# Kernel optimization log

Hardware: AMD Instinct MI355X
Metric: run time of the kernel (lower is better)

Reference implementation:

```python
import jax, jax.numpy as jnp
import numpy as np
import math

B, L, D_MODEL, H = 8, 3072, 1024, 16
E = D_MODEL // H                      # d_keys = d_values = 64
FACTOR = 1
TOP_K = int(FACTOR * math.log(L))     # = 8 delay taps


def setup_inputs() -> dict:
    key = jax.random.key(0)
    ks = jax.random.split(key, 11)
    s = 0.02
    return {
        "queries": jax.random.normal(ks[0], (B, L, D_MODEL), jnp.float32),
        "keys":    jax.random.normal(ks[1], (B, L, D_MODEL), jnp.float32),
        "values":  jax.random.normal(ks[2], (B, L, D_MODEL), jnp.float32),
        "Wq": jax.random.normal(ks[3], (D_MODEL, D_MODEL), jnp.float32) * s,
        "bq": jnp.zeros((D_MODEL,), jnp.float32),
        "Wk": jax.random.normal(ks[4], (D_MODEL, D_MODEL), jnp.float32) * s,
        "bk": jnp.zeros((D_MODEL,), jnp.float32),
        "Wv": jax.random.normal(ks[5], (D_MODEL, D_MODEL), jnp.float32) * s,
        "bv": jnp.zeros((D_MODEL,), jnp.float32),
        "Wo": jax.random.normal(ks[6], (D_MODEL, D_MODEL), jnp.float32) * s,
        "bo": jnp.zeros((D_MODEL,), jnp.float32),
    }


def reference(queries, keys, values, Wq, bq, Wk, bk, Wv, bv, Wo, bo):
    # Q/K/V projections -> [B, L, H, E]
    q = (queries @ Wq + bq).reshape(B, L, H, E)
    k = (keys    @ Wk + bk).reshape(B, L, H, E)
    v = (values  @ Wv + bv).reshape(B, L, H, E)

    # -> [B, H, E, L], correlate along time via FFT
    qh = q.transpose(0, 2, 3, 1)
    kh = k.transpose(0, 2, 3, 1)
    vh = v.transpose(0, 2, 3, 1)
    qf = jnp.fft.rfft(qh, axis=-1)
    kf = jnp.fft.rfft(kh, axis=-1)
    corr = jnp.fft.irfft(qf * jnp.conj(kf), n=L, axis=-1)  # [B, H, E, L]

    # per-batch top-k delay selection on head/channel-averaged correlation
    mean_value = corr.mean(axis=(1, 2))                    # [B, L]
    weights, delay = jax.lax.top_k(mean_value, TOP_K)      # [B, K]
    tmp_corr = jax.nn.softmax(weights, axis=-1)            # [B, K]

    # time-delay aggregation: circular gather per selected delay, weighted sum
    init_index = jnp.arange(L)
    agg = jnp.zeros_like(vh)
    for i in range(TOP_K):  # small static loop over top-k taps
        idx = (init_index[None, :] + delay[:, i:i + 1]) % L            # [B, L]
        idx4 = jnp.broadcast_to(idx[:, None, None, :], vh.shape)       # [B,H,E,L]
        pattern = jnp.take_along_axis(vh, idx4, axis=-1)
        agg = agg + pattern * tmp_corr[:, i][:, None, None, None]

    # back to [B, L, H*E], output projection
    V = agg.transpose(0, 3, 1, 2).reshape(B, L, H * E)
    return V @ Wo + bo
```

## Files before the change

### kernel.cpp

```cpp
#include <hip/hip_runtime.h>
#include <math.h>

#define BSZ 8
#define LEN 3072
#define DM 1024
#define TOPK 8

typedef __attribute__((ext_vector_type(8))) short short8;
typedef __attribute__((ext_vector_type(4))) float f32x4;

__device__ __forceinline__ unsigned short f2bf(float x) {
    unsigned int u = __builtin_bit_cast(unsigned int, x);
    u += 0x7fffu + ((u >> 16) & 1u);
    return (unsigned short)(u >> 16);
}
__device__ __forceinline__ float bf2f(unsigned short h) {
    unsigned int u = ((unsigned int)h) << 16;
    return __builtin_bit_cast(float, u);
}
__device__ __forceinline__ void gl_lds16(const void* g, void* l) {
    __builtin_amdgcn_global_load_lds(
        (const __attribute__((address_space(1))) unsigned int*)g,
        (__attribute__((address_space(3))) unsigned int*)l, 16, 0, 0);
}

#define GBM 128
#define GBN 128
#define GBK 16

__global__ __launch_bounds__(256) void gemm_f32(const float* __restrict__ A,
    const float* __restrict__ B, float* __restrict__ C, int M, int N, int K)
{
    __shared__ float As[GBK][GBM];
    __shared__ float Bs[GBK][GBN];
    const int tid = threadIdx.x;
    const int tx = tid & 15, ty = tid >> 4;
    const size_t m0 = (size_t)blockIdx.y * GBM;
    const size_t n0 = (size_t)blockIdx.x * GBN;
    const int arow = tid >> 2, acol = (tid & 3) << 2;
    const int brow = tid >> 5, bcol = (tid & 31) << 2;

    float acc[8][8];
#pragma unroll
    for (int i = 0; i < 8; i++)
#pragma unroll
        for (int j = 0; j < 8; j++) acc[i][j] = 0.f;

    const float* Ap0 = A + (m0 + arow) * (size_t)K + acol;
    const float* Ap1 = A + (m0 + arow + 64) * (size_t)K + acol;
    const float* Bp0 = B + (size_t)brow * N + n0 + bcol;
    const float* Bp1 = B + (size_t)(brow + 8) * N + n0 + bcol;

    for (int k0 = 0; k0 < K; k0 += GBK) {
        float4 a0 = *(const float4*)(Ap0 + k0);
        float4 a1 = *(const float4*)(Ap1 + k0);
        float4 b0 = *(const float4*)(Bp0 + (size_t)k0 * N);
        float4 b1 = *(const float4*)(Bp1 + (size_t)k0 * N);
        __syncthreads();
        As[acol + 0][arow] = a0.x; As[acol + 1][arow] = a0.y;
        As[acol + 2][arow] = a0.z; As[acol + 3][arow] = a0.w;
        As[acol + 0][arow + 64] = a1.x; As[acol + 1][arow + 64] = a1.y;
        As[acol + 2][arow + 64] = a1.z; As[acol + 3][arow + 64] = a1.w;
        *(float4*)&Bs[brow][bcol] = b0;
        *(float4*)&Bs[brow + 8][bcol] = b1;
        __syncthreads();
#pragma unroll
        for (int kk = 0; kk < GBK; kk++) {
            float av[8], bv[8];
            *(float4*)&av[0] = *(const float4*)&As[kk][ty * 8];
            *(float4*)&av[4] = *(const float4*)&As[kk][ty * 8 + 4];
            *(float4*)&bv[0] = *(const float4*)&Bs[kk][tx * 8];
            *(float4*)&bv[4] = *(const float4*)&Bs[kk][tx * 8 + 4];
#pragma unroll
            for (int i = 0; i < 8; i++)
#pragma unroll
                for (int j = 0; j < 8; j++)
                    acc[i][j] = fmaf(av[i], bv[j], acc[i][j]);
        }
    }
#pragma unroll
    for (int i = 0; i < 8; i++) {
        size_t row = m0 + (size_t)(ty * 8 + i);
        float* Cp = C + row * N + n0 + tx * 8;
#pragma unroll
        for (int j = 0; j < 8; j++) Cp[j] = acc[i][j];
    }
}

__global__ __launch_bounds__(256) void gemm_split_zT(
    const unsigned short* __restrict__ Khi, const unsigned short* __restrict__ Klo,
    const unsigned short* __restrict__ AhiT, const unsigned short* __restrict__ AloT,
    const float* __restrict__ bias, float* __restrict__ zT, int M, int N, int K)
{
    __shared__ unsigned short Ah[128 * 32];
    __shared__ unsigned short Al[128 * 32];
    __shared__ unsigned short Bh[128 * 32];
    __shared__ unsigned short Bl[128 * 32];
    const int tid = threadIdx.x;
    const int lane = tid & 63;
    const int wv = tid >> 6;
    const int wm = wv >> 1, wn = wv & 1;
    const int l16 = lane & 15, quad = lane >> 4;
    const size_t m0 = (size_t)blockIdx.y * 128;
    const size_t n0 = (size_t)blockIdx.x * 128;

    const int s0 = tid, s1 = tid + 256;
    const size_t oA0 = (m0 + (s0 >> 2)) * (size_t)K + (s0 & 3) * 8;
    const size_t oA1 = (m0 + (s1 >> 2)) * (size_t)K + (s1 & 3) * 8;
    const size_t oB0 = (n0 + (s0 >> 2)) * (size_t)K + (s0 & 3) * 8;
    const size_t oB1 = (n0 + (s1 >> 2)) * (size_t)K + (s1 & 3) * 8;

    f32x4 acc[4][4];
#pragma unroll
    for (int i = 0; i < 4; i++)
#pragma unroll
        for (int j = 0; j < 4; j++) acc[i][j] = (f32x4){0.f, 0.f, 0.f, 0.f};

    for (int k0 = 0; k0 < K; k0 += 32) {
        __syncthreads();
        gl_lds16(Khi + oA0 + k0, &Ah[s0 * 8]);
        gl_lds16(Khi + oA1 + k0, &Ah[s1 * 8]);
        gl_lds16(Klo + oA0 + k0, &Al[s0 * 8]);
        gl_lds16(Klo + oA1 + k0, &Al[s1 * 8]);
        gl_lds16(AhiT + oB0 + k0, &Bh[s0 * 8]);
        gl_lds16(AhiT + oB1 + k0, &Bh[s1 * 8]);
        gl_lds16(AloT + oB0 + k0, &Bl[s0 * 8]);
        gl_lds16(AloT + oB1 + k0, &Bl[s1 * 8]);
        __syncthreads();
        short8 ah[4], al[4], bh[4], bl[4];
#pragma unroll
        for (int mi = 0; mi < 4; mi++) {
            int off = (wm * 64 + mi * 16 + l16) * 32 + quad * 8;
            ah[mi] = *(const short8*)&Ah[off];
            al[mi] = *(const short8*)&Al[off];
        }
#pragma unroll
        for (int ni = 0; ni < 4; ni++) {
            int off = (wn * 64 + ni * 16 + l16) * 32 + quad * 8;
            bh[ni] = *(const short8*)&Bh[off];
            bl[ni] = *(const short8*)&Bl[off];
        }
#pragma unroll
        for (int mi = 0; mi < 4; mi++)
#pragma unroll
            for (int ni = 0; ni < 4; ni++) {
                acc[mi][ni] = __builtin_amdgcn_mfma_f32_16x16x32_bf16(
                    ah[mi], bh[ni], acc[mi][ni], 0, 0, 0);
                acc[mi][ni] = __builtin_amdgcn_mfma_f32_16x16x32_bf16(
                    ah[mi], bl[ni], acc[mi][ni], 0, 0, 0);
                acc[mi][ni] = __builtin_amdgcn_mfma_f32_16x16x32_bf16(
                    al[mi], bh[ni], acc[mi][ni], 0, 0, 0);
            }
    }

    const int b = (int)(m0 / LEN);
    const int t0 = (int)(m0 % LEN);
#pragma unroll
    for (int mi = 0; mi < 4; mi++) {
#pragma unroll
        for (int ni = 0; ni < 4; ni++) {
            int c = (int)n0 + wn * 64 + ni * 16 + l16;
            int t = t0 + wm * 64 + mi * 16 + quad * 4;
            float bb = bias[c];
            float* zp = zT + ((size_t)b * DM + c) * LEN + t;
#pragma unroll
            for (int r = 0; r < 4; r++) zp[r] = acc[mi][ni][r] + bb;
        }
    }
}

__global__ __launch_bounds__(256) void gemm_bf16(const unsigned short* __restrict__ A,
    const unsigned short* __restrict__ Bt, const float* __restrict__ bias,
    void* __restrict__ C, int M, int N, int K, int cmode)
{
    __shared__ unsigned short As[128 * 32];
    __shared__ unsigned short Bs[128 * 32];
    const int tid = threadIdx.x;
    const int lane = tid & 63;
    const int wv = tid >> 6;
    const int wm = wv >> 1, wn = wv & 1;
    const int l16 = lane & 15, quad = lane >> 4;
    const size_t m0 = (size_t)blockIdx.y * 128;
    const size_t n0 = (size_t)blockIdx.x * 128;

    const int s0 = tid, s1 = tid + 256;
    const unsigned short* gA0 = A + (m0 + (s0 >> 2)) * (size_t)K + (s0 & 3) * 8;
    const unsigned short* gA1 = A + (m0 + (s1 >> 2)) * (size_t)K + (s1 & 3) * 8;
    const unsigned short* gB0 = Bt + (n0 + (s0 >> 2)) * (size_t)K + (s0 & 3) * 8;
    const unsigned short* gB1 = Bt + (n0 + (s1 >> 2)) * (size_t)K + (s1 & 3) * 8;
    unsigned short* lA0 = &As[s0 * 8];
    unsigned short* lA1 = &As[s1 * 8];
    unsigned short* lB0 = &Bs[s0 * 8];
    unsigned short* lB1 = &Bs[s1 * 8];

    f32x4 acc[4][4];
#pragma unroll
    for (int i = 0; i < 4; i++)
#pragma unroll
        for (int j = 0; j < 4; j++) acc[i][j] = (f32x4){0.f, 0.f, 0.f, 0.f};

    for (int k0 = 0; k0 < K; k0 += 32) {
        __syncthreads();
        gl_lds16(gA0 + k0, lA0);
        gl_lds16(gA1 + k0, lA1);
        gl_lds16(gB0 + k0, lB0);
        gl_lds16(gB1 + k0, lB1);
        __syncthreads();
        short8 af[4], bf[4];
#pragma unroll
        for (int mi = 0; mi < 4; mi++)
            af[mi] = *(const short8*)&As[(wm * 64 + mi * 16 + l16) * 32 + quad * 8];
#pragma unroll
        for (int ni = 0; ni < 4; ni++)
            bf[ni] = *(const short8*)&Bs[(wn * 64 + ni * 16 + l16) * 32 + quad * 8];
#pragma unroll
        for (int mi = 0; mi < 4; mi++)
#pragma unroll
            for (int ni = 0; ni < 4; ni++)
                acc[mi][ni] = __builtin_amdgcn_mfma_f32_16x16x32_bf16(
                    af[mi], bf[ni], acc[mi][ni], 0, 0, 0);
    }

#pragma unroll
    for (int mi = 0; mi < 4; mi++) {
#pragma unroll
        for (int ni = 0; ni < 4; ni++) {
            int gm = (int)m0 + wm * 64 + mi * 16 + quad * 4;
            int gn = (int)n0 + wn * 64 + ni * 16 + l16;
            float bb = bias ? bias[gn] : 0.f;
#pragma unroll
            for (int r = 0; r < 4; r++) {
                float v = acc[mi][ni][r] + bb;
                if (cmode == 0)
                    ((float*)C)[(size_t)(gm + r) * N + gn] = v;
                else
                    ((unsigned short*)C)[(size_t)(gm + r) * N + gn] = f2bf(v);
            }
        }
    }
}

__global__ __launch_bounds__(256) void transpose_bld(const float* __restrict__ in,
                                                     float* __restrict__ out)
{
    __shared__ float tile[32][33];
    int b = blockIdx.z;
    int d0 = blockIdx.x * 32, t0 = blockIdx.y * 32;
    int tx = threadIdx.x & 31, ty = threadIdx.x >> 5;
    const float* ip = in + (size_t)b * LEN * DM;
    float* op = out + (size_t)b * DM * LEN;
#pragma unroll
    for (int r = 0; r < 4; r++)
        tile[ty * 4 + r][tx] = ip[(size_t)(t0 + ty * 4 + r) * DM + d0 + tx];
    __syncthreads();
#pragma unroll
    for (int r = 0; r < 4; r++)
        op[(size_t)(d0 + ty * 4 + r) * LEN + t0 + tx] = tile[tx][ty * 4 + r];
}

__global__ __launch_bounds__(256) void transpose_1024(const float* __restrict__ in,
                                                      float* __restrict__ out)
{
    __shared__ float tile[32][33];
    int bx = blockIdx.x & 31, by = blockIdx.x >> 5;
    int tx = threadIdx.x & 31, tq = threadIdx.x >> 5;
#pragma unroll
    for (int r = 0; r < 4; r++)
        tile[tq * 4 + r][tx] = in[(size_t)(by * 32 + tq * 4 + r) * 1024 + bx * 32 + tx];
    __syncthreads();
#pragma unroll
    for (int r = 0; r < 4; r++)
        out[(size_t)(bx * 32 + tq * 4 + r) * 1024 + by * 32 + tx] = tile[tx][tq * 4 + r];
}

__global__ __launch_bounds__(256) void transpose_w_bf16(const float* __restrict__ in,
                                                        unsigned short* __restrict__ out)
{
    __shared__ float tile[32][33];
    int bx = blockIdx.x & 31, by = blockIdx.x >> 5;
    int tx = threadIdx.x & 31, tq = threadIdx.x >> 5;
#pragma unroll
    for (int r = 0; r < 4; r++)
        tile[tq * 4 + r][tx] = in[(size_t)(by * 32 + tq * 4 + r) * 1024 + bx * 32 + tx];
    __syncthreads();
#pragma unroll
    for (int r = 0; r < 4; r++)
        out[(size_t)(bx * 32 + tq * 4 + r) * 1024 + by * 32 + tx] = f2bf(tile[tx][tq * 4 + r]);
}

__global__ __launch_bounds__(256) void transpose_w_split(const float* __restrict__ in,
    unsigned short* __restrict__ hi, unsigned short* __restrict__ lo)
{
    __shared__ float tile[32][33];
    int bx = blockIdx.x & 31, by = blockIdx.x >> 5;
    int tx = threadIdx.x & 31, tq = threadIdx.x >> 5;
#pragma unroll
    for (int r = 0; r < 4; r++)
        tile[tq * 4 + r][tx] = in[(size_t)(by * 32 + tq * 4 + r) * 1024 + bx * 32 + tx];
    __syncthreads();
#pragma unroll
    for (int r = 0; r < 4; r++) {
        float x = tile[tx][tq * 4 + r];
        unsigned short h = f2bf(x);
        unsigned short l = f2bf(x - bf2f(h));
        size_t o = (size_t)(bx * 32 + tq * 4 + r) * 1024 + by * 32 + tx;
        hi[o] = h; lo[o] = l;
    }
}

__global__ __launch_bounds__(256) void split_bf16(const float* __restrict__ in,
    unsigned short* __restrict__ hi, unsigned short* __restrict__ lo, size_t n)
{
    size_t i = ((size_t)blockIdx.x * 256 + threadIdx.x) * 4;
    if (i >= n) return;
    float4 v = *(const float4*)(in + i);
    ushort4 h, l;
    h.x = f2bf(v.x); l.x = f2bf(v.x - bf2f(h.x));
    h.y = f2bf(v.y); l.y = f2bf(v.y - bf2f(h.y));
    h.z = f2bf(v.z); l.z = f2bf(v.z - bf2f(h.z));
    h.w = f2bf(v.w); l.w = f2bf(v.w - bf2f(h.w));
    *(ushort4*)(hi + i) = h;
    *(ushort4*)(lo + i) = l;
}

__global__ __launch_bounds__(256) void conv_bf16(const float* __restrict__ in,
                                                 unsigned short* __restrict__ out, size_t n)
{
    size_t i = ((size_t)blockIdx.x * 256 + threadIdx.x) * 4;
    if (i >= n) return;
    float4 v = *(const float4*)(in + i);
    ushort4 o;
    o.x = f2bf(v.x); o.y = f2bf(v.y); o.z = f2bf(v.z); o.w = f2bf(v.w);
    *(ushort4*)(out + i) = o;
}

__global__ __launch_bounds__(256) void bz_kernel(const float* __restrict__ bk,
    const float* __restrict__ WqT, float* __restrict__ bz)
{
    int j = blockIdx.x * 256 + threadIdx.x;
    float s = 0.f;
    for (int d = 0; d < 1024; d++) s = fmaf(bk[d], WqT[(size_t)d * 1024 + j], s);
    bz[j] = s;
}

__global__ void zero_f32(float* __restrict__ p, int n)
{
    int i = blockIdx.x * 256 + threadIdx.x;
    if (i < n) p[i] = 0.f;
}

__device__ __forceinline__ int swz(int i) { return i ^ ((i >> 4) & 15); }

__device__ __forceinline__ float2 cmul(float2 a, float2 b) {
    return make_float2(a.x * b.x - a.y * b.y, a.x * b.y + a.y * b.x);
}

__device__ __forceinline__ void fft3072_r4(float2* __restrict__ bufA,
                                           float2* __restrict__ bufB,
                                           const float2* __restrict__ tw,
                                           const float2* __restrict__ t3, int tid)
{
    float2* src = bufA;
    float2* dst = bufB;
#pragma unroll
    for (int s = 0; s < 10; s += 2) {
        const int st = 1 << s;
        const int q = tid & (st - 1);
        const int p = tid >> s;
        const float2 wA = tw[p << s];
        const float2 w2 = tw[p << (s + 1)];
        const int io = q + (p << (s + 2));
#pragma unroll
        for (int k = 0; k < 3; k++) {
            const int base = k << 10;
            float2 a1 = src[swz(base + tid)];
            float2 a2 = src[swz(base + tid + 256)];
            float2 b1 = src[swz(base + tid + 512)];
            float2 b2 = src[swz(base + tid + 768)];
            float2 uA0 = make_float2(a1.x + b1.x, a1.y + b1.y);
            float2 d1  = make_float2(a1.x - b1.x, a1.y - b1.y);
            float2 uA1 = cmul(d1, wA);
            float2 uB0 = make_float2(a2.x + b2.x, a2.y + b2.y);
            float2 d2  = make_float2(a2.x - b2.x, a2.y - b2.y);
            float2 e   = cmul(d2, wA);
            float2 uB1 = make_float2(e.y, -e.x);
            float2 o0 = make_float2(uA0.x + uB0.x, uA0.y + uB0.y);
            float2 o1 = make_float2(uA1.x + uB1.x, uA1.y + uB1.y);
            float2 e2 = make_float2(uA0.x - uB0.x, uA0.y - uB0.y);
            float2 e3 = make_float2(uA1.x - uB1.x, uA1.y - uB1.y);
            dst[swz(base + io)] = o0;
            dst[swz(base + io + st)] = o1;
            dst[swz(base + io + 2 * st)] = cmul(e2, w2);
            dst[swz(base + io + 3 * st)] = cmul(e3, w2);
        }
        __syncthreads();
        float2* t = src; src = dst; dst = t;
    }
    const float OMR = -0.5f, OMI = -0.86602540378443864676f;
#pragma unroll
    for (int j = 0; j < 4; j++) {
        int k2 = tid + (j << 8);
        float2 y0 = src[swz(k2)];
        float2 y1 = src[swz(1024 + k2)];
        float2 y2 = src[swz(2048 + k2)];
        float2 w1 = t3[k2];
        float2 w2c = make_float2(w1.x * w1.x - w1.y * w1.y, 2.f * w1.x * w1.y);
        float2 u1 = cmul(y1, w1);
        float2 u2 = cmul(y2, w2c);
        dst[swz(k2)] = make_float2(y0.x + u1.x + u2.x, y0.y + u1.y + u2.y);
        dst[swz(1024 + k2)] = make_float2(
            y0.x + (OMR * u1.x - OMI * u1.y) + (OMR * u2.x + OMI * u2.y),
            y0.y + (OMR * u1.y + OMI * u1.x) + (OMR * u2.y - OMI * u2.x));
        dst[swz(2048 + k2)] = make_float2(
            y0.x + (OMR * u1.x + OMI * u1.y) + (OMR * u2.x - OMI * u2.y),
            y0.y + (OMR * u1.y - OMI * u1.x) + (OMR * u2.y + OMI * u2.x));
    }
    __syncthreads();
}

__global__ __launch_bounds__(256) void fft_corr(const float* __restrict__ qT,
    const float* __restrict__ zT, float* __restrict__ S)
{
    __shared__ float2 bufA[3072], bufB[3072];
    __shared__ float2 tw[512], t3[1024];
    const int tid = threadIdx.x;
    const int b = blockIdx.x >> 6;
    const int c0 = (blockIdx.x & 63) << 4;
    const float TWO_PI = 6.28318530717958647692f;
    for (int j = tid; j < 512; j += 256) {
        float s, c; sincosf(-TWO_PI * (float)j / 1024.f, &s, &c);
        tw[j] = make_float2(c, s);
    }
    for (int j = tid; j < 1024; j += 256) {
        float s, c; sincosf(-TWO_PI * (float)j / 3072.f, &s, &c);
        t3[j] = make_float2(c, s);
    }
    float pR[12], pI[12];
#pragma unroll
    for (int j = 0; j < 12; j++) { pR[j] = 0.f; pI[j] = 0.f; }
    __syncthreads();

    for (int ci = 0; ci < 16; ci++) {
        int c = c0 + ci;
        const float* qp = qT + ((size_t)b * DM + c) * LEN;
        const float* zp = zT + ((size_t)b * DM + c) * LEN;
        for (int t = tid; t < 3072; t += 256) {
            float qv = qp[t];
            float zv = zp[t];
            int t1 = t % 3, t2 = t / 3;
            bufA[swz(t1 * 1024 + t2)] = make_float2(qv, zv);
        }
        __syncthreads();
        fft3072_r4(bufA, bufB, tw, t3, tid);
#pragma unroll
        for (int j = 0; j < 12; j++) {
            int f = tid + (j << 8);
            int fc = (f == 0) ? 0 : 3072 - f;
            float2 Wf = bufA[swz(f)];
            float2 Wc = bufA[swz(fc)];
            float WcI = -Wc.y;
            float qR = 0.5f * (Wf.x + Wc.x), qI = 0.5f * (Wf.y + WcI);
            float dR = Wf.x - Wc.x, dI = Wf.y - WcI;
            float zR = 0.5f * dI, zI = -0.5f * dR;
            pR[j] += qR * zR + qI * zI;
            pI[j] += qI * zR - qR * zI;
        }
        __syncthreads();
    }
    float* Sb = S + (size_t)b * 3072 * 2;
#pragma unroll
    for (int j = 0; j < 12; j++) {
        int f = tid + (j << 8);
        atomicAdd(&Sb[f * 2 + 0], pR[j]);
        atomicAdd(&Sb[f * 2 + 1], pI[j]);
    }
}

__global__ __launch_bounds__(256) void ifft_mean(const float* __restrict__ S,
                                                 float* __restrict__ mv)
{
    __shared__ float2 bufA[3072], bufB[3072];
    __shared__ float2 tw[512], t3[1024];
    const int tid = threadIdx.x;
    const int b = blockIdx.x;
    const float TWO_PI = 6.28318530717958647692f;
    for (int j = tid; j < 512; j += 256) {
        float s, c; sincosf(-TWO_PI * (float)j / 1024.f, &s, &c);
        tw[j] = make_float2(c, s);
    }
    for (int j = tid; j < 1024; j += 256) {
        float s, c; sincosf(-TWO_PI * (float)j / 3072.f, &s, &c);
        t3[j] = make_float2(c, s);
    }
    __syncthreads();
    for (int t = tid; t < 3072; t += 256) {
        float sR = S[((size_t)b * 3072 + t) * 2 + 0];
        float sI = S[((size_t)b * 3072 + t) * 2 + 1];
        int t1 = t % 3, t2 = t / 3;
        bufA[swz(t1 * 1024 + t2)] = make_float2(sR, -sI);
    }
    __syncthreads();
    fft3072_r4(bufA, bufB, tw, t3, tid);
    const float scale = 1.f / (3072.f * 1024.f);
    for (int t = tid; t < 3072; t += 256)
        mv[(size_t)b * 3072 + t] = bufA[swz(t)].x * scale;
}

__global__ __launch_bounds__(256) void topk_softmax(const float* __restrict__ mv,
    float* __restrict__ wout, int* __restrict__ dout)
{
    const int b = blockIdx.x, tid = threadIdx.x;
    __shared__ float v[3072];
    __shared__ float rv[256];
    __shared__ int   ri[256];
    __shared__ float topv[TOPK];
    __shared__ int   topi[TOPK];
    for (int t = tid; t < 3072; t += 256) v[t] = mv[(size_t)b * 3072 + t];
    __syncthreads();
    for (int it = 0; it < TOPK; it++) {
        float best = -3.0e38f; int bi = 0;
        for (int t = tid; t < 3072; t += 256) {
            float x = v[t];
            if (x > best) { best = x; bi = t; }
        }
        rv[tid] = best; ri[tid] = bi;
        __syncthreads();
        for (int off = 128; off > 0; off >>= 1) {
            if (tid < off) {
                float ov = rv[tid + off]; int oi = ri[tid + off];
                if (ov > rv[tid] || (ov == rv[tid] && oi < ri[tid])) {
                    rv[tid] = ov; ri[tid] = oi;
                }
            }
            __syncthreads();
        }
        if (tid == 0) { topv[it] = rv[0]; topi[it] = ri[0]; v[ri[0]] = -3.0e38f; }
        __syncthreads();
    }
    if (tid == 0) {
        float m = topv[0];
        float e[TOPK]; float ssum = 0.f;
        for (int i = 0; i < TOPK; i++) { e[i] = expf(topv[i] - m); ssum += e[i]; }
        for (int i = 0; i < TOPK; i++) {
            wout[b * TOPK + i] = e[i] / ssum;
            dout[b * TOPK + i] = topi[i];
        }
    }
}

__global__ __launch_bounds__(256) void agg_bf16(const unsigned short* __restrict__ V,
    const float* __restrict__ w, const int* __restrict__ d,
    unsigned short* __restrict__ agg)
{
    size_t gid = (size_t)blockIdx.x * 256 + threadIdx.x;
    int c8 = (int)(gid & 127);
    size_t rest = gid >> 7;
    int t = (int)(rest % LEN);
    int b = (int)(rest / LEN);
    float acc[8];
#pragma unroll
    for (int j = 0; j < 8; j++) acc[j] = 0.f;
#pragma unroll
    for (int i = 0; i < TOPK; i++) {
        float wi = w[b * TOPK + i];
        int r = t + d[b * TOPK + i];
        if (r >= LEN) r -= LEN;
        const unsigned short* vp = V + ((size_t)b * LEN + r) * DM + c8 * 8;
        uint4 raw = *(const uint4*)vp;
        unsigned int uu[4] = {raw.x, raw.y, raw.z, raw.w};
#pragma unroll
        for (int k = 0; k < 4; k++) {
            acc[2 * k]     = fmaf(wi, bf2f((unsigned short)(uu[k] & 0xffff)), acc[2 * k]);
            acc[2 * k + 1] = fmaf(wi, bf2f((unsigned short)(uu[k] >> 16)), acc[2 * k + 1]);
        }
    }
    unsigned int ou[4];
#pragma unroll
    for (int k = 0; k < 4; k++)
        ou[k] = (unsigned int)f2bf(acc[2 * k]) | ((unsigned int)f2bf(acc[2 * k + 1]) << 16);
    uint4 o = {ou[0], ou[1], ou[2], ou[3]};
    *(uint4*)(agg + gid * 8) = o;
}

extern "C" void kernel_launch(void* const* d_in, const int* in_sizes, int n_in,
                              void* d_out, int out_size, void* d_ws, size_t ws_size,
                              hipStream_t stream)
{
    const float* queries = (const float*)d_in[0];
    const float* keys    = (const float*)d_in[1];
    const float* values  = (const float*)d_in[2];
    const float* Wq = (const float*)d_in[3];
    const float* Wk = (const float*)d_in[5];
    const float* bk = (const float*)d_in[6];
    const float* Wv = (const float*)d_in[7];
    const float* bv = (const float*)d_in[8];
    const float* Wo = (const float*)d_in[9];
    const float* bo = (const float*)d_in[10];
    float* out = (float*)d_out;

    char* ws = (char*)d_ws;
    size_t off = 0;
    auto alloc = [&](size_t bytes) -> char* {
        char* p = ws + off;
        off += (bytes + 255) & ~(size_t)255;
        return p;
    };
    const size_t BLD = (size_t)BSZ * LEN * DM;
    float* WqT  = (float*)alloc((size_t)1024 * 1024 * 4);
    float* Amat = (float*)alloc((size_t)1024 * 1024 * 4);
    unsigned short* AhiT = (unsigned short*)alloc((size_t)1024 * 1024 * 2);
    unsigned short* AloT = (unsigned short*)alloc((size_t)1024 * 1024 * 2);
    float* bz   = (float*)alloc(1024 * 4);
    float* S    = (float*)alloc((size_t)BSZ * 3072 * 2 * 4);
    float* mv   = (float*)alloc((size_t)BSZ * 3072 * 4);
    float* wsm  = (float*)alloc(BSZ * TOPK * 4);
    int*   dly  = (int*)alloc(BSZ * TOPK * 4);
    unsigned short* WvT = (unsigned short*)alloc((size_t)1024 * 1024 * 2);
    unsigned short* WoT = (unsigned short*)alloc((size_t)1024 * 1024 * 2);
    char* bigA = alloc(BLD * 4);
    char* bigB = alloc(BLD * 4);
    unsigned short* khi = (unsigned short*)bigA;
    unsigned short* klo = (unsigned short*)(bigA + BLD * 2);
    float* qT = (float*)bigA;
    float* zT = (float*)bigB;
    unsigned short* vb16 = (unsigned short*)bigA;
    unsigned short* aggb = (unsigned short*)(bigA + BLD * 2);
    unsigned short* Vb   = (unsigned short*)bigB;

    const int BL = BSZ * LEN;

    transpose_1024<<<1024, 256, 0, stream>>>(Wq, WqT);
    gemm_f32<<<dim3(8, 8), 256, 0, stream>>>(Wk, WqT, Amat, 1024, 1024, 1024);
    bz_kernel<<<4, 256, 0, stream>>>(bk, WqT, bz);
    transpose_w_split<<<1024, 256, 0, stream>>>(Amat, AhiT, AloT);
    split_bf16<<<(int)((BLD / 4 + 255) / 256), 256, 0, stream>>>(keys, khi, klo, BLD);
    gemm_split_zT<<<dim3(8, 192), 256, 0, stream>>>(khi, klo, AhiT, AloT, bz, zT,
                                                    BL, 1024, 1024);
    transpose_bld<<<dim3(32, 96, 8), 256, 0, stream>>>(queries, qT);
    zero_f32<<<(BSZ * 3072 * 2 + 255) / 256, 256, 0, stream>>>(S, BSZ * 3072 * 2);
    fft_corr<<<BSZ * 64, 256, 0, stream>>>(qT, zT, S);
    ifft_mean<<<BSZ, 256, 0, stream>>>(S, mv);
    topk_softmax<<<BSZ, 256, 0, stream>>>(mv, wsm, dly);

    conv_bf16<<<(int)((BLD / 4 + 255) / 256), 256, 0, stream>>>(values, vb16, BLD);
    transpose_w_bf16<<<1024, 256, 0, stream>>>(Wv, WvT);
    transpose_w_bf16<<<1024, 256, 0, stream>>>(Wo, WoT);
    gemm_bf16<<<dim3(8, 192), 256, 0, stream>>>(vb16, WvT, bv, Vb, BL, 1024, 1024, 1);
    agg_bf16<<<(int)(((size_t)BL * 128) / 256), 256, 0, stream>>>(Vb, wsm, dly, aggb);
    gemm_bf16<<<dim3(8, 192), 256, 0, stream>>>(aggb, WoT, bo, out, BL, 1024, 1024, 0);
}
```

Baseline: 1.054 ms.

## Split-K weight GEMM, XCD tile swizzle, register twiddles, half-spectrum FFT accumulation

```diff
diff --git a/kernel.cpp b/kernel.cpp
--- a/kernel.cpp
+++ b/kernel.cpp
@@ -28,8 +28,8 @@
 #define GBN 128
 #define GBK 16
 
-__global__ __launch_bounds__(256) void gemm_f32(const float* __restrict__ A,
-    const float* __restrict__ B, float* __restrict__ C, int M, int N, int K)
+__global__ __launch_bounds__(256) void gemm_f32_sk(const float* __restrict__ A,
+    const float* __restrict__ B, float* __restrict__ P, int M, int N, int K)
 {
     __shared__ float As[GBK][GBM];
     __shared__ float Bs[GBK][GBN];
@@ -37,6 +37,8 @@
     const int tx = tid & 15, ty = tid >> 4;
     const size_t m0 = (size_t)blockIdx.y * GBM;
     const size_t n0 = (size_t)blockIdx.x * GBN;
+    const int ksl = K >> 2;
+    const int kb = blockIdx.z * ksl, ke = kb + ksl;
     const int arow = tid >> 2, acol = (tid & 3) << 2;
     const int brow = tid >> 5, bcol = (tid & 31) << 2;
 
@@ -51,7 +53,7 @@
     const float* Bp0 = B + (size_t)brow * N + n0 + bcol;
     const float* Bp1 = B + (size_t)(brow + 8) * N + n0 + bcol;
 
-    for (int k0 = 0; k0 < K; k0 += GBK) {
+    for (int k0 = kb; k0 < ke; k0 += GBK) {
         float4 a0 = *(const float4*)(Ap0 + k0);
         float4 a1 = *(const float4*)(Ap1 + k0);
         float4 b0 = *(const float4*)(Bp0 + (size_t)k0 * N);
@@ -78,12 +80,38 @@
                     acc[i][j] = fmaf(av[i], bv[j], acc[i][j]);
         }
     }
+    float* Pz = P + (size_t)blockIdx.z * M * N;
 #pragma unroll
     for (int i = 0; i < 8; i++) {
         size_t row = m0 + (size_t)(ty * 8 + i);
-        float* Cp = C + row * N + n0 + tx * 8;
+        float* Cp = Pz + row * N + n0 + tx * 8;
 #pragma unroll
         for (int j = 0; j < 8; j++) Cp[j] = acc[i][j];
+    }
+}
+
+__global__ __launch_bounds__(256) void reduce4_f32(const float* __restrict__ P,
+                                                   float* __restrict__ C, int n)
+{
+    int i = (blockIdx.x * 256 + threadIdx.x) * 4;
+    if (i >= n) return;
+    float4 a = *(const float4*)(P + i);
+    float4 b = *(const float4*)(P + (size_t)n + i);
+    float4 c = *(const float4*)(P + 2 * (size_t)n + i);
+    float4 d = *(const float4*)(P + 3 * (size_t)n + i);
+    float4 o = {a.x + b.x + c.x + d.x, a.y + b.y + c.y + d.y,
+                a.z + b.z + c.z + d.z, a.w + b.w + c.w + d.w};
+    *(float4*)(C + i) = o;
+}
+
+__device__ __forceinline__ void xcd_tile(int& bx, int& by) {
+    int nbx = gridDim.x, nby = gridDim.y;
+    int nwg = nbx * nby;
+    int flat = by * nbx + bx;
+    if (!(nwg & 7)) {
+        int sw = (flat & 7) * (nwg >> 3) + (flat >> 3);
+        bx = sw % nbx;
+        by = sw / nbx;
     }
 }
 
@@ -101,8 +129,10 @@
     const int wv = tid >> 6;
     const int wm = wv >> 1, wn = wv & 1;
     const int l16 = lane & 15, quad = lane >> 4;
-    const size_t m0 = (size_t)blockIdx.y * 128;
-    const size_t n0 = (size_t)blockIdx.x * 128;
+    int bx = blockIdx.x, by = blockIdx.y;
+    xcd_tile(bx, by);
+    const size_t m0 = (size_t)by * 128;
+    const size_t n0 = (size_t)bx * 128;
 
     const int s0 = tid, s1 = tid + 256;
     const size_t oA0 = (m0 + (s0 >> 2)) * (size_t)K + (s0 & 3) * 8;
@@ -180,8 +210,10 @@
     const int wv = tid >> 6;
     const int wm = wv >> 1, wn = wv & 1;
     const int l16 = lane & 15, quad = lane >> 4;
-    const size_t m0 = (size_t)blockIdx.y * 128;
-    const size_t n0 = (size_t)blockIdx.x * 128;
+    int bx = blockIdx.x, by = blockIdx.y;
+    xcd_tile(bx, by);
+    const size_t m0 = (size_t)by * 128;
+    const size_t n0 = (size_t)bx * 128;
 
     const int s0 = tid, s1 = tid + 256;
     const unsigned short* gA0 = A + (m0 + (s0 >> 2)) * (size_t)K + (s0 & 3) * 8;
@@ -355,10 +387,33 @@
     return make_float2(a.x * b.x - a.y * b.y, a.x * b.y + a.y * b.x);
 }
 
+struct TwRegs {
+    float2 wA[5], w2[5], w1[4], w2c[4];
+};
+
+__device__ __forceinline__ void make_tw(TwRegs& T, int tid)
+{
+    const float TWO_PI = 6.28318530717958647692f;
+#pragma unroll
+    for (int si = 0; si < 5; si++) {
+        int s = si * 2;
+        int a = (tid >> s) << s;
+        float sv, cv; sincosf(-TWO_PI * (float)a / 1024.f, &sv, &cv);
+        T.wA[si] = make_float2(cv, sv);
+        T.w2[si] = make_float2(cv * cv - sv * sv, 2.f * cv * sv);
+    }
+#pragma unroll
+    for (int j = 0; j < 4; j++) {
+        int k2 = tid + (j << 8);
+        float sv, cv; sincosf(-TWO_PI * (float)k2 / 3072.f, &sv, &cv);
+        T.w1[j] = make_float2(cv, sv);
+        T.w2c[j] = make_float2(cv * cv - sv * sv, 2.f * cv * sv);
+    }
+}
+
 __device__ __forceinline__ void fft3072_r4(float2* __restrict__ bufA,
                                            float2* __restrict__ bufB,
-                                           const float2* __restrict__ tw,
-                                           const float2* __restrict__ t3, int tid)
+                                           const TwRegs& T, int tid)
 {
     float2* src = bufA;
     float2* dst = bufB;
@@ -367,8 +422,8 @@
         const int st = 1 << s;
         const int q = tid & (st - 1);
         const int p = tid >> s;
-        const float2 wA = tw[p << s];
-        const float2 w2 = tw[p << (s + 1)];
+        const float2 wA = T.wA[s >> 1];
+        const float2 w2 = T.w2[s >> 1];
         const int io = q + (p << (s + 2));
 #pragma unroll
         for (int k = 0; k < 3; k++) {
@@ -403,8 +458,8 @@
         float2 y0 = src[swz(k2)];
         float2 y1 = src[swz(1024 + k2)];
         float2 y2 = src[swz(2048 + k2)];
-        float2 w1 = t3[k2];
-        float2 w2c = make_float2(w1.x * w1.x - w1.y * w1.y, 2.f * w1.x * w1.y);
+        float2 w1 = T.w1[j];
+        float2 w2c = T.w2c[j];
         float2 u1 = cmul(y1, w1);
         float2 u2 = cmul(y2, w2c);
         dst[swz(k2)] = make_float2(y0.x + u1.x + u2.x, y0.y + u1.y + u2.y);
@@ -418,29 +473,21 @@
     __syncthreads();
 }
 
-__global__ __launch_bounds__(256) void fft_corr(const float* __restrict__ qT,
+__global__ __launch_bounds__(256, 3) void fft_corr(const float* __restrict__ qT,
     const float* __restrict__ zT, float* __restrict__ S)
 {
     __shared__ float2 bufA[3072], bufB[3072];
-    __shared__ float2 tw[512], t3[1024];
     const int tid = threadIdx.x;
-    const int b = blockIdx.x >> 6;
-    const int c0 = (blockIdx.x & 63) << 4;
-    const float TWO_PI = 6.28318530717958647692f;
-    for (int j = tid; j < 512; j += 256) {
-        float s, c; sincosf(-TWO_PI * (float)j / 1024.f, &s, &c);
-        tw[j] = make_float2(c, s);
-    }
-    for (int j = tid; j < 1024; j += 256) {
-        float s, c; sincosf(-TWO_PI * (float)j / 3072.f, &s, &c);
-        t3[j] = make_float2(c, s);
-    }
-    float pR[12], pI[12];
-#pragma unroll
-    for (int j = 0; j < 12; j++) { pR[j] = 0.f; pI[j] = 0.f; }
-    __syncthreads();
-
-    for (int ci = 0; ci < 16; ci++) {
+    const int b = blockIdx.x >> 7;
+    const int c0 = (blockIdx.x & 127) << 3;
+    TwRegs T;
+    make_tw(T, tid);
+    float pR[6], pI[6];
+#pragma unroll
+    for (int j = 0; j < 6; j++) { pR[j] = 0.f; pI[j] = 0.f; }
+    float eR = 0.f, eI = 0.f;
+
+    for (int ci = 0; ci < 8; ci++) {
         int c = c0 + ci;
         const float* qp = qT + ((size_t)b * DM + c) * LEN;
         const float* zp = zT + ((size_t)b * DM + c) * LEN;
@@ -451,9 +498,9 @@
             bufA[swz(t1 * 1024 + t2)] = make_float2(qv, zv);
         }
         __syncthreads();
-        fft3072_r4(bufA, bufB, tw, t3, tid);
-#pragma unroll
-        for (int j = 0; j < 12; j++) {
+        fft3072_r4(bufA, bufB, T, tid);
+#pragma unroll
+        for (int j = 0; j < 6; j++) {
             int f = tid + (j << 8);
             int fc = (f == 0) ? 0 : 3072 - f;
             float2 Wf = bufA[swz(f)];
@@ -465,42 +512,47 @@
             pR[j] += qR * zR + qI * zI;
             pI[j] += qI * zR - qR * zI;
         }
+        if (tid == 0) {
+            float2 Wf = bufA[swz(1536)];
+            float qR = Wf.x, qI = 0.f;
+            float dI = 2.f * Wf.y;
+            float zR = 0.5f * dI, zI = 0.f;
+            eR += qR * zR + qI * zI;
+            eI += qI * zR - qR * zI;
+        }
         __syncthreads();
     }
     float* Sb = S + (size_t)b * 3072 * 2;
 #pragma unroll
-    for (int j = 0; j < 12; j++) {
+    for (int j = 0; j < 6; j++) {
         int f = tid + (j << 8);
         atomicAdd(&Sb[f * 2 + 0], pR[j]);
         atomicAdd(&Sb[f * 2 + 1], pI[j]);
     }
+    if (tid == 0) {
+        atomicAdd(&Sb[1536 * 2 + 0], eR);
+        atomicAdd(&Sb[1536 * 2 + 1], eI);
+    }
 }
 
 __global__ __launch_bounds__(256) void ifft_mean(const float* __restrict__ S,
                                                  float* __restrict__ mv)
 {
     __shared__ float2 bufA[3072], bufB[3072];
-    __shared__ float2 tw[512], t3[1024];
     const int tid = threadIdx.x;
     const int b = blockIdx.x;
-    const float TWO_PI = 6.28318530717958647692f;
-    for (int j = tid; j < 512; j += 256) {
-        float s, c; sincosf(-TWO_PI * (float)j / 1024.f, &s, &c);
-        tw[j] = make_float2(c, s);
-    }
-    for (int j = tid; j < 1024; j += 256) {
-        float s, c; sincosf(-TWO_PI * (float)j / 3072.f, &s, &c);
-        t3[j] = make_float2(c, s);
+    TwRegs T;
+    make_tw(T, tid);
+    for (int t = tid; t < 3072; t += 256) {
+        int tt = (t <= 1536) ? t : 3072 - t;
+        float sR = S[((size_t)b * 3072 + tt) * 2 + 0];
+        float sI = S[((size_t)b * 3072 + tt) * 2 + 1];
+        float im = (t > 1536) ? sI : -sI;
+        int t1 = t % 3, t2 = t / 3;
+        bufA[swz(t1 * 1024 + t2)] = make_float2(sR, im);
     }
     __syncthreads();
-    for (int t = tid; t < 3072; t += 256) {
-        float sR = S[((size_t)b * 3072 + t) * 2 + 0];
-        float sI = S[((size_t)b * 3072 + t) * 2 + 1];
-        int t1 = t % 3, t2 = t / 3;
-        bufA[swz(t1 * 1024 + t2)] = make_float2(sR, -sI);
-    }
-    __syncthreads();
-    fft3072_r4(bufA, bufB, tw, t3, tid);
+    fft3072_r4(bufA, bufB, T, tid);
     const float scale = 1.f / (3072.f * 1024.f);
     for (int t = tid; t < 3072; t += 256)
         mv[(size_t)b * 3072 + t] = bufA[swz(t)].x * scale;
@@ -623,6 +675,7 @@
     unsigned short* klo = (unsigned short*)(bigA + BLD * 2);
     float* qT = (float*)bigA;
     float* zT = (float*)bigB;
+    float* Apart = (float*)bigB;
     unsigned short* vb16 = (unsigned short*)bigA;
     unsigned short* aggb = (unsigned short*)(bigA + BLD * 2);
     unsigned short* Vb   = (unsigned short*)bigB;
@@ -630,7 +683,8 @@
     const int BL = BSZ * LEN;
 
     transpose_1024<<<1024, 256, 0, stream>>>(Wq, WqT);
-    gemm_f32<<<dim3(8, 8), 256, 0, stream>>>(Wk, WqT, Amat, 1024, 1024, 1024);
+    gemm_f32_sk<<<dim3(8, 8, 4), 256, 0, stream>>>(Wk, WqT, Apart, 1024, 1024, 1024);
+    reduce4_f32<<<1024, 256, 0, stream>>>(Apart, Amat, 1024 * 1024);
     bz_kernel<<<4, 256, 0, stream>>>(bk, WqT, bz);
     transpose_w_split<<<1024, 256, 0, stream>>>(Amat, AhiT, AloT);
     split_bf16<<<(int)((BLD / 4 + 255) / 256), 256, 0, stream>>>(keys, khi, klo, BLD);
@@ -638,7 +692,7 @@
                                                     BL, 1024, 1024);
     transpose_bld<<<dim3(32, 96, 8), 256, 0, stream>>>(queries, qT);
     zero_f32<<<(BSZ * 3072 * 2 + 255) / 256, 256, 0, stream>>>(S, BSZ * 3072 * 2);
-    fft_corr<<<BSZ * 64, 256, 0, stream>>>(qT, zT, S);
+    fft_corr<<<BSZ * 128, 256, 0, stream>>>(qT, zT, S);
     ifft_mean<<<BSZ, 256, 0, stream>>>(S, mv);
     topk_softmax<<<BSZ, 256, 0, stream>>>(mv, wsm, dly);
 
```

Measured after the change: 1.117 ms. 5.9% more time.
